# Kernel tuning notes

Hardware: AMD Instinct MI355X
Metric: run time of the kernel (lower is better)

The kernel has to match this reference:

```python
import jax, jax.numpy as jnp
import numpy as np

N_NODES = 100000
N_EDGES = 1600000
F_IN = 128
HID = 128


def setup_inputs() -> dict:
    key = jax.random.key(0)
    ks = jax.random.split(key, 10)
    x = jax.random.normal(ks[0], (N_NODES, F_IN), dtype=jnp.float32)
    edge_index = jax.random.randint(ks[1], (2, N_EDGES), 0, N_NODES, dtype=jnp.int64)
    edge_weight = jax.random.uniform(ks[2], (N_EDGES,), dtype=jnp.float32)
    # Glorot-style params for the three GCNConv layers (conv_mid reused twice)
    W_in = jax.random.normal(ks[3], (F_IN, HID), dtype=jnp.float32) / np.sqrt(F_IN)
    b_in = jnp.zeros((HID,), dtype=jnp.float32)
    W_mid = jax.random.normal(ks[4], (HID, HID), dtype=jnp.float32) / np.sqrt(HID)
    b_mid = jnp.zeros((HID,), dtype=jnp.float32)
    W_fin = jax.random.normal(ks[5], (HID, 1), dtype=jnp.float32) / np.sqrt(HID)
    b_fin = jnp.zeros((1,), dtype=jnp.float32)
    return {"x": x, "edge_index": edge_index, "edge_weight": edge_weight,
            "W_in": W_in, "b_in": b_in, "W_mid": W_mid, "b_mid": b_mid,
            "W_fin": W_fin, "b_fin": b_fin}


def _gcn_norm(edge_index, edge_weight, n_nodes):
    """PyG GCNConv normalization with implicit self-loops (weight 1).
    Returns (edge_norm [E], self_norm [N]) where self_norm = 1/deg."""
    dst = edge_index[1]
    deg = jax.ops.segment_sum(edge_weight, dst, num_segments=n_nodes) + 1.0
    dinv = jnp.where(deg > 0, jax.lax.rsqrt(deg), 0.0)  # deg^-1/2
    edge_norm = dinv[edge_index[0]] * edge_weight * dinv[dst]
    self_norm = dinv * dinv  # self-loop: dinv[i] * 1 * dinv[i]
    return edge_norm, self_norm


def _gcn_conv(x, edge_index, edge_norm, self_norm, W, b, n_nodes):
    h = x @ W  # [N, out]
    msgs = edge_norm[:, None] * h[edge_index[0]]  # [E, out]
    agg = jax.ops.segment_sum(msgs, edge_index[1], num_segments=n_nodes)
    return agg + self_norm[:, None] * h + b


def reference(x, edge_index, edge_weight, W_in, b_in, W_mid, b_mid, W_fin, b_fin):
    n = x.shape[0]
    edge_norm, self_norm = _gcn_norm(edge_index, edge_weight, n)
    h = jax.nn.relu(_gcn_conv(x, edge_index, edge_norm, self_norm, W_in, b_in, n))
    h = jax.nn.relu(_gcn_conv(h, edge_index, edge_norm, self_norm, W_mid, b_mid, n))
    h = jax.nn.relu(_gcn_conv(h, edge_index, edge_norm, self_norm, W_mid, b_mid, n))
    out = _gcn_conv(h, edge_index, edge_norm, self_norm, W_fin, b_fin, n)
    return out  # [N, 1]
```

## Files before the change

kernel.cpp:

```cpp
#include <hip/hip_runtime.h>
#include <stdint.h>

#define N_NODES 100000
#define N_EDGES 1600000
#define F 128
#define CBN 512
#define NCBK 196
#define CHUNK 4096
#define BUFCAP 10240

typedef _Float16 f16;
typedef _Float16 f16x4 __attribute__((ext_vector_type(4)));
typedef _Float16 f16x8 __attribute__((ext_vector_type(8)));
typedef float f32x4 __attribute__((ext_vector_type(4)));

__device__ inline float unpackw(unsigned int p) {
    unsigned short b = (unsigned short)(p & 0x7FFF);
    return (float)__builtin_bit_cast(f16, b);
}


__global__ void k_zero0(int* gcur, unsigned int* edges) {
    int i = threadIdx.x;
    if (i < NCBK) gcur[i] = 0;
    if (i >= 248) edges[(size_t)NCBK * BUFCAP + (i - 248)] = 0u;
}


__launch_bounds__(256)
__global__ void k_binA(const int* __restrict__ ei, const float* __restrict__ w,
                       int* __restrict__ gcur, int2* __restrict__ stage, int e) {
    __shared__ int hist[256];
    __shared__ int bst[257];
    __shared__ int gb[256];
    __shared__ int ls[256];
    __shared__ int rec[CHUNK];
    __shared__ int meta[CHUNK];
    int tid = threadIdx.x;
    int base = blockIdx.x * CHUNK;
    int cnt = min(CHUNK, e - base);
    hist[tid] = 0;
    __syncthreads();

    int ew_[16], mr_[16];
    int nloc = 0;
    if (cnt == CHUNK) {
#pragma unroll
        for (int k = 0; k < 16; k++) {
            int i = base + tid + k * 256;
            int s = ei[i];
            int d = ei[N_EDGES + i];
            f16 hw = (f16)w[i];
            unsigned short wb = __builtin_bit_cast(unsigned short, hw);
            ew_[k] = (int)(((unsigned int)s << 15) | (wb & 0x7FFF));
            int cb = d >> 9;
            int local = d & (CBN - 1);
            int r = atomicAdd(&hist[cb], 1);
            mr_[k] = (cb << 22) | (local << 13) | r;
        }
        nloc = 16;
    } else {
        for (int i = tid; i < cnt; i += 256) {
            int s = ei[base + i];
            int d = ei[N_EDGES + base + i];
            f16 hw = (f16)w[base + i];
            unsigned short wb = __builtin_bit_cast(unsigned short, hw);
            ew_[nloc] = (int)(((unsigned int)s << 15) | (wb & 0x7FFF));
            int cb = d >> 9;
            int local = d & (CBN - 1);
            int r = atomicAdd(&hist[cb], 1);
            mr_[nloc] = (cb << 22) | (local << 13) | r;
            nloc++;
        }
    }
    __syncthreads();
    int v = hist[tid];
    ls[tid] = v;
    __syncthreads();
    for (int off = 1; off < 256; off <<= 1) {
        int t = (tid >= off) ? ls[tid - off] : 0;
        __syncthreads();
        ls[tid] += t;
        __syncthreads();
    }
    bst[tid] = ls[tid] - v;
    if (tid == 255) bst[256] = ls[255];
    __syncthreads();
    for (int k = 0; k < nloc; k++) {
        int m = mr_[k];
        int cb = m >> 22;
        int pos = bst[cb] + (m & 0x1FFF);
        rec[pos] = ew_[k];
        meta[pos] = (cb << 9) | ((m >> 13) & 0x1FF);
    }
    __syncthreads();
    if (tid < NCBK) {
        int c = bst[tid + 1] - bst[tid];
        gb[tid] = c ? atomicAdd(&gcur[tid], c) : 0;
    }
    __syncthreads();
    for (int j = tid; j < cnt; j += 256) {
        int m = meta[j];
        int cb = m >> 9;
        stage[(size_t)cb * BUFCAP + gb[cb] + (j - bst[cb])] = make_int2(m & 511, rec[j]);
    }
}

__launch_bounds__(256)
__global__ void k_binB(const int2* __restrict__ stage, const int* __restrict__ gcur,
                       unsigned int* __restrict__ edges, int2* __restrict__ row2,
                       float* __restrict__ dinv) {
    __shared__ int cnt[CBN];
    __shared__ int ex[CBN + 1];
    __shared__ int cur[CBN];
    __shared__ int ls[256];
    __shared__ unsigned int buf[BUFCAP];
    int tid = threadIdx.x;
    int cb = blockIdx.x;
    int n0 = cb * CBN;
    int nn = min(CBN, N_NODES - n0);
    size_t sbase = (size_t)cb * BUFCAP;
    int ecnt = gcur[cb];
    cnt[tid] = 0;
    cnt[tid + 256] = 0;
    __syncthreads();
    for (int j = tid; j < ecnt; j += 256)
        atomicAdd(&cnt[stage[sbase + j].x], 1);
    __syncthreads();
    int a = cnt[2 * tid], b = cnt[2 * tid + 1];
    int s = a + b;
    ls[tid] = s;
    __syncthreads();
    for (int off = 1; off < 256; off <<= 1) {
        int t = (tid >= off) ? ls[tid - off] : 0;
        __syncthreads();
        ls[tid] += t;
        __syncthreads();
    }
    int bx = ls[tid] - s;
    ex[2 * tid] = bx;
    ex[2 * tid + 1] = bx + a;
    cur[2 * tid] = bx;
    cur[2 * tid + 1] = bx + a;
    if (tid == 255) ex[512] = ls[255];
    __syncthreads();
    for (int l = tid; l < nn; l += 256)
        row2[n0 + l] = make_int2((int)sbase + ex[l], (int)sbase + ex[l + 1]);
    for (int j = tid; j < ecnt; j += 256) {
        int2 r = stage[sbase + j];
        int p = atomicAdd(&cur[r.x], 1);
        buf[p] = (unsigned int)r.y;
    }
    __syncthreads();
    for (int j = tid; j < ecnt; j += 256)
        edges[sbase + j] = buf[j];
    for (int l = tid; l < nn; l += 256) {
        int lo = ex[l];
        int h2 = ex[l + 1];
        float sm = 1.0f;
        for (int j = lo; j < h2; j++) sm += unpackw(buf[j]);
        dinv[n0 + l] = rsqrtf(sm);
    }
}


__global__ void k_wt2(const float* __restrict__ Wa, const float* __restrict__ Wb,
                      f16* __restrict__ Wta, f16* __restrict__ Wtb) {
    const float* W = blockIdx.x ? Wb : Wa;
    f16* Wt = blockIdx.x ? Wtb : Wta;
    int t = threadIdx.x;
#pragma unroll
    for (int it = 0; it < 64; it++) {
        int idx = t + it * 256;
        int k = idx >> 7, n = idx & 127;
        Wt[n * 128 + k] = (f16)W[idx];
    }
}


#define LDK 136

__launch_bounds__(256, 2)
__global__ void k_gemm16(const f16* __restrict__ A, const f16* __restrict__ Wt,
                         const float* __restrict__ dinv, f16* __restrict__ H, int nrows) {
    __shared__ f16 Ws[128 * LDK];
    int tid = threadIdx.x;
    int r0 = blockIdx.x * 128;
    int wave = tid >> 6;
    int lane = tid & 63;
    int lrow = lane & 15;
    int quad = lane >> 4;

    f16x8 a[2][4];
#pragma unroll
    for (int mt = 0; mt < 2; mt++) {
        int row = r0 + wave * 32 + mt * 16 + lrow;
#pragma unroll
        for (int kc = 0; kc < 4; kc++) {
            if (row < nrows)
                a[mt][kc] = *(const f16x8*)&A[(size_t)row * F + kc * 32 + quad * 8];
            else
                a[mt][kc] = (f16x8){};
        }
    }
#pragma unroll
    for (int it = 0; it < 8; it++) {
        int c = tid + it * 256;
        int rw = c >> 4;
        int off = (c & 15) * 8;
        *(f16x8*)&Ws[rw * LDK + off] = *(const f16x8*)&Wt[rw * 128 + off];
    }
    __syncthreads();

    f32x4 acc[2][8] = {};
#pragma unroll
    for (int kc = 0; kc < 4; kc++) {
        f16x8 b[8];
#pragma unroll
        for (int nt = 0; nt < 8; nt++)
            b[nt] = *(const f16x8*)&Ws[(nt * 16 + lrow) * LDK + kc * 32 + quad * 8];
#pragma unroll
        for (int nt = 0; nt < 8; nt++) {
            acc[0][nt] = __builtin_amdgcn_mfma_f32_16x16x32_f16(a[0][kc], b[nt], acc[0][nt], 0, 0, 0);
            acc[1][nt] = __builtin_amdgcn_mfma_f32_16x16x32_f16(a[1][kc], b[nt], acc[1][nt], 0, 0, 0);
        }
    }
    __syncthreads();
#pragma unroll
    for (int mt = 0; mt < 2; mt++) {
#pragma unroll
        for (int r = 0; r < 4; r++) {
            int lr = wave * 32 + mt * 16 + quad * 4 + r;
            int grow = r0 + lr;
            float dv = (grow < nrows) ? dinv[grow] : 0.f;
#pragma unroll
            for (int nt = 0; nt < 8; nt++)
                Ws[lr * 132 + nt * 16 + lrow] = (f16)(acc[mt][nt][r] * dv);
        }
    }
    __syncthreads();
#pragma unroll
    for (int it = 0; it < 8; it++) {
        int c = it * 256 + tid;
        int rw = c >> 4;
        int col = (c & 15) * 8;
        int grow = r0 + rw;
        if (grow < nrows)
            *(f16x8*)&H[(size_t)grow * F + col] = *(const f16x8*)&Ws[rw * 132 + col];
    }
}

__launch_bounds__(256, 2)
__global__ void k_gemmf(const float* __restrict__ A, const f16* __restrict__ Wt,
                        const float* __restrict__ dinv, f16* __restrict__ H, int nrows) {
    __shared__ f16 Ws[128 * LDK];
    int tid = threadIdx.x;
    int r0 = blockIdx.x * 128;
    int wave = tid >> 6;
    int lane = tid & 63;
    int lrow = lane & 15;
    int quad = lane >> 4;

    f16x8 a[2][4];
#pragma unroll
    for (int mt = 0; mt < 2; mt++) {
        int row = r0 + wave * 32 + mt * 16 + lrow;
#pragma unroll
        for (int kc = 0; kc < 4; kc++) {
            if (row < nrows) {
                float4 lo = *(const float4*)&A[(size_t)row * F + kc * 32 + quad * 8];
                float4 hi = *(const float4*)&A[(size_t)row * F + kc * 32 + quad * 8 + 4];
                f16x8 f;
                f[0] = (f16)lo.x; f[1] = (f16)lo.y; f[2] = (f16)lo.z; f[3] = (f16)lo.w;
                f[4] = (f16)hi.x; f[5] = (f16)hi.y; f[6] = (f16)hi.z; f[7] = (f16)hi.w;
                a[mt][kc] = f;
            } else {
                a[mt][kc] = (f16x8){};
            }
        }
    }
#pragma unroll
    for (int it = 0; it < 8; it++) {
        int c = tid + it * 256;
        int rw = c >> 4;
        int off = (c & 15) * 8;
        *(f16x8*)&Ws[rw * LDK + off] = *(const f16x8*)&Wt[rw * 128 + off];
    }
    __syncthreads();

    f32x4 acc[2][8] = {};
#pragma unroll
    for (int kc = 0; kc < 4; kc++) {
        f16x8 b[8];
#pragma unroll
        for (int nt = 0; nt < 8; nt++)
            b[nt] = *(const f16x8*)&Ws[(nt * 16 + lrow) * LDK + kc * 32 + quad * 8];
#pragma unroll
        for (int nt = 0; nt < 8; nt++) {
            acc[0][nt] = __builtin_amdgcn_mfma_f32_16x16x32_f16(a[0][kc], b[nt], acc[0][nt], 0, 0, 0);
            acc[1][nt] = __builtin_amdgcn_mfma_f32_16x16x32_f16(a[1][kc], b[nt], acc[1][nt], 0, 0, 0);
        }
    }
    __syncthreads();
#pragma unroll
    for (int mt = 0; mt < 2; mt++) {
#pragma unroll
        for (int r = 0; r < 4; r++) {
            int lr = wave * 32 + mt * 16 + quad * 4 + r;
            int grow = r0 + lr;
            float dv = (grow < nrows) ? dinv[grow] : 0.f;
#pragma unroll
            for (int nt = 0; nt < 8; nt++)
                Ws[lr * 132 + nt * 16 + lrow] = (f16)(acc[mt][nt][r] * dv);
        }
    }
    __syncthreads();
#pragma unroll
    for (int it = 0; it < 8; it++) {
        int c = it * 256 + tid;
        int rw = c >> 4;
        int col = (c & 15) * 8;
        int grow = r0 + rw;
        if (grow < nrows)
            *(f16x8*)&H[(size_t)grow * F + col] = *(const f16x8*)&Ws[rw * 132 + col];
    }
}


__launch_bounds__(256)
__global__ void k_agg(const f16* __restrict__ H16, const int2* __restrict__ row2,
                      const unsigned int* __restrict__ edges,
                      const float* __restrict__ dinv, const float* __restrict__ bias,
                      f16* __restrict__ out, int n) {
    int node = blockIdx.x * 16 + (threadIdx.x >> 4);
    if (node >= n) return;
    int sub = threadIdx.x & 15;
    int2 rr = row2[node];
    int beg = rr.x, end = rr.y;
    float acc0[8] = {}, acc1[8] = {}, acc2[8] = {}, acc3[8] = {};
    for (int t = (beg & ~3); t < end; t += 8) {
        uint4 ea = *(const uint4*)&edges[t];
        uint4 eb = *(const uint4*)&edges[t + 4];
        unsigned int e[8] = {ea.x, ea.y, ea.z, ea.w, eb.x, eb.y, eb.z, eb.w};
        float w[8];
        unsigned int srcw[8];
#pragma unroll
        for (int k = 0; k < 8; k++) {
            bool live = (t + k >= beg) && (t + k < end);
            w[k] = live ? unpackw(e[k]) : 0.f;
            srcw[k] = (t + k < end) ? e[k] : ea.x;
        }
        f16x8 v[8];
#pragma unroll
        for (int k = 0; k < 8; k++)
            v[k] = *(const f16x8*)&H16[(size_t)(srcw[k] >> 15) * F + sub * 8];
#pragma unroll
        for (int j = 0; j < 8; j++) {
            acc0[j] = fmaf(w[0], (float)v[0][j], acc0[j]);
            acc1[j] = fmaf(w[1], (float)v[1][j], acc1[j]);
            acc2[j] = fmaf(w[2], (float)v[2][j], acc2[j]);
            acc3[j] = fmaf(w[3], (float)v[3][j], acc3[j]);
            acc0[j] = fmaf(w[4], (float)v[4][j], acc0[j]);
            acc1[j] = fmaf(w[5], (float)v[5][j], acc1[j]);
            acc2[j] = fmaf(w[6], (float)v[6][j], acc2[j]);
            acc3[j] = fmaf(w[7], (float)v[7][j], acc3[j]);
        }
    }
    float dd = dinv[node];
    f16x8 h = *(const f16x8*)&H16[(size_t)node * F + sub * 8];
    float4 b0 = *(const float4*)&bias[sub * 8];
    float4 b1 = *(const float4*)&bias[sub * 8 + 4];
    float bb[8] = {b0.x, b0.y, b0.z, b0.w, b1.x, b1.y, b1.z, b1.w};
    f16x8 o;
#pragma unroll
    for (int j = 0; j < 8; j++) {
        float a = acc0[j] + acc1[j] + acc2[j] + acc3[j] + (float)h[j];
        o[j] = (f16)fmaxf(fmaf(dd, a, bb[j]), 0.f);
    }
    *(f16x8*)&out[(size_t)node * F + sub * 8] = o;
}

__launch_bounds__(256)
__global__ void k_agg_dot(const f16* __restrict__ H16, const int2* __restrict__ row2,
                          const unsigned int* __restrict__ edges,
                          const float* __restrict__ dinv, const float* __restrict__ bias,
                          const float* __restrict__ Wf, float* __restrict__ sout, int n) {
    int node = blockIdx.x * 16 + (threadIdx.x >> 4);
    if (node >= n) return;
    int sub = threadIdx.x & 15;
    int2 rr = row2[node];
    int beg = rr.x, end = rr.y;
    float acc0[8] = {}, acc1[8] = {}, acc2[8] = {}, acc3[8] = {};
    for (int t = (beg & ~3); t < end; t += 8) {
        uint4 ea = *(const uint4*)&edges[t];
        uint4 eb = *(const uint4*)&edges[t + 4];
        unsigned int e[8] = {ea.x, ea.y, ea.z, ea.w, eb.x, eb.y, eb.z, eb.w};
        float w[8];
        unsigned int srcw[8];
#pragma unroll
        for (int k = 0; k < 8; k++) {
            bool live = (t + k >= beg) && (t + k < end);
            w[k] = live ? unpackw(e[k]) : 0.f;
            srcw[k] = (t + k < end) ? e[k] : ea.x;
        }
        f16x8 v[8];
#pragma unroll
        for (int k = 0; k < 8; k++)
            v[k] = *(const f16x8*)&H16[(size_t)(srcw[k] >> 15) * F + sub * 8];
#pragma unroll
        for (int j = 0; j < 8; j++) {
            acc0[j] = fmaf(w[0], (float)v[0][j], acc0[j]);
            acc1[j] = fmaf(w[1], (float)v[1][j], acc1[j]);
            acc2[j] = fmaf(w[2], (float)v[2][j], acc2[j]);
            acc3[j] = fmaf(w[3], (float)v[3][j], acc3[j]);
            acc0[j] = fmaf(w[4], (float)v[4][j], acc0[j]);
            acc1[j] = fmaf(w[5], (float)v[5][j], acc1[j]);
            acc2[j] = fmaf(w[6], (float)v[6][j], acc2[j]);
            acc3[j] = fmaf(w[7], (float)v[7][j], acc3[j]);
        }
    }
    float dd = dinv[node];
    f16x8 h = *(const f16x8*)&H16[(size_t)node * F + sub * 8];
    float4 b0 = *(const float4*)&bias[sub * 8];
    float4 b1 = *(const float4*)&bias[sub * 8 + 4];
    float bb[8] = {b0.x, b0.y, b0.z, b0.w, b1.x, b1.y, b1.z, b1.w};
    float4 w0v = *(const float4*)&Wf[sub * 8];
    float4 w1v = *(const float4*)&Wf[sub * 8 + 4];
    float ww[8] = {w0v.x, w0v.y, w0v.z, w0v.w, w1v.x, w1v.y, w1v.z, w1v.w};
    float p = 0.f;
#pragma unroll
    for (int j = 0; j < 8; j++) {
        float a = acc0[j] + acc1[j] + acc2[j] + acc3[j] + (float)h[j];
        p += fmaxf(fmaf(dd, a, bb[j]), 0.f) * ww[j];
    }
    p += __shfl_xor(p, 8, 64);
    p += __shfl_xor(p, 4, 64);
    p += __shfl_xor(p, 2, 64);
    p += __shfl_xor(p, 1, 64);
    if (sub == 0) sout[node] = dd * p;
}

__global__ void k_aggs(const float* __restrict__ s, const int2* __restrict__ row2,
                       const unsigned int* __restrict__ edges,
                       const float* __restrict__ dinv, const float* __restrict__ bf,
                       float* __restrict__ out, int n) {
    int i = blockIdx.x * blockDim.x + threadIdx.x;
    if (i >= n) return;
    float dd = dinv[i];
    float ae = s[i];
    int2 rr = row2[i];
    for (int j = rr.x; j < rr.y; j++) {
        unsigned int p = edges[j];
        ae = fmaf(unpackw(p), s[p >> 15], ae);
    }
    out[i] = fmaf(dd, ae, bf[0]);
}


extern "C" void kernel_launch(void* const* d_in, const int* in_sizes, int n_in,
                              void* d_out, int out_size, void* d_ws, size_t ws_size,
                              hipStream_t stream) {
    const float* x    = (const float*)d_in[0];
    const int*   ei   = (const int*)d_in[1];
    const float* ew   = (const float*)d_in[2];
    const float* Win  = (const float*)d_in[3];
    const float* bin  = (const float*)d_in[4];
    const float* Wmid = (const float*)d_in[5];
    const float* bmid = (const float*)d_in[6];
    const float* Wfin = (const float*)d_in[7];
    const float* bfin = (const float*)d_in[8];
    float* out = (float*)d_out;

    char* ws = (char*)d_ws;
    size_t off = 0;
    auto alloc = [&](size_t bytes) -> char* {
        char* p = ws + off;
        off = (off + bytes + 255) & ~(size_t)255;
        return p;
    };
    float* dinv  = (float*)alloc((size_t)N_NODES * 4);
    int2*  row2  = (int2*)alloc((size_t)N_NODES * 8);
    unsigned int* edges = (unsigned int*)alloc(((size_t)NCBK * BUFCAP + 8) * 4);
    int*   gcur  = (int*)alloc(256 * 4);
    f16*   wtin  = (f16*)alloc(128 * 128 * 2);
    f16*   wtmid = (f16*)alloc(128 * 128 * 2);
    f16*   H16   = (f16*)alloc((size_t)N_NODES * F * 2);
    f16*   AB16  = (f16*)alloc((size_t)N_NODES * F * 2);
    int2* stage = (int2*)H16;
    float* sbuf = (float*)AB16;

    dim3 b256(256);
    int gN = (N_NODES + 255) / 256;
    int gW = (N_NODES + 15) / 16;
    int gG = (N_NODES + 127) / 128;
    int gA = (N_EDGES + CHUNK - 1) / CHUNK;

    hipLaunchKernelGGL(k_zero0, dim3(1), b256, 0, stream, gcur, edges);
    hipLaunchKernelGGL(k_binA, dim3(gA), b256, 0, stream, ei, ew, gcur, stage, N_EDGES);
    hipLaunchKernelGGL(k_binB, dim3(NCBK), b256, 0, stream, stage, gcur, edges, row2, dinv);
    hipLaunchKernelGGL(k_wt2, dim3(2), b256, 0, stream, Win, Wmid, wtin, wtmid);

    hipLaunchKernelGGL(k_gemmf, dim3(gG), b256, 0, stream, x, wtin, dinv, H16, N_NODES);
    hipLaunchKernelGGL(k_agg, dim3(gW), b256, 0, stream, H16, row2, edges, dinv, bin, AB16, N_NODES);
    hipLaunchKernelGGL(k_gemm16, dim3(gG), b256, 0, stream, AB16, wtmid, dinv, H16, N_NODES);
    hipLaunchKernelGGL(k_agg, dim3(gW), b256, 0, stream, H16, row2, edges, dinv, bmid, AB16, N_NODES);
    hipLaunchKernelGGL(k_gemm16, dim3(gG), b256, 0, stream, AB16, wtmid, dinv, H16, N_NODES);
    hipLaunchKernelGGL(k_agg_dot, dim3(gW), b256, 0, stream, H16, row2, edges, dinv, bmid, Wfin, sbuf, N_NODES);
    hipLaunchKernelGGL(k_aggs, dim3(gN), b256, 0, stream, sbuf, row2, edges, dinv, bfin, out, N_NODES);
}
```

Before: 387.4 us.

## Fuse neighbor aggregation with next-layer GEMM and merge zeroing into weight transpose

Replaces the separate aggregation and f16 GEMM kernels with one kernel that aggregates 128 nodes into shared memory, then multiplies by the next layer's weights with MFMA and writes the scaled result. This avoids writing the aggregated activations to global memory and reading them back, and cuts kernel launches. The zeroing kernel is folded into the weight-transpose launch as an extra block. The trade-off is lower gather parallelism: each block processes 128 nodes, with 8 sequential node iterations per thread group, and the fused kernel uses more registers and LDS, which could reduce latency hiding for the irregular gathers.

```diff
diff --git a/kernel.cpp b/kernel.cpp
--- a/kernel.cpp
+++ b/kernel.cpp
@@ -19,12 +19,6 @@
     return (float)__builtin_bit_cast(f16, b);
 }
 
-
-__global__ void k_zero0(int* gcur, unsigned int* edges) {
-    int i = threadIdx.x;
-    if (i < NCBK) gcur[i] = 0;
-    if (i >= 248) edges[(size_t)NCBK * BUFCAP + (i - 248)] = 0u;
-}
 
 
 __launch_bounds__(256)
@@ -165,10 +159,16 @@
 
 
 __global__ void k_wt2(const float* __restrict__ Wa, const float* __restrict__ Wb,
-                      f16* __restrict__ Wta, f16* __restrict__ Wtb) {
+                      f16* __restrict__ Wta, f16* __restrict__ Wtb,
+                      int* __restrict__ gcur, unsigned int* __restrict__ edges) {
+    int t = threadIdx.x;
+    if (blockIdx.x == 2) {
+        if (t < NCBK) gcur[t] = 0;
+        if (t >= 248) edges[(size_t)NCBK * BUFCAP + (t - 248)] = 0u;
+        return;
+    }
     const float* W = blockIdx.x ? Wb : Wa;
     f16* Wt = blockIdx.x ? Wtb : Wta;
-    int t = threadIdx.x;
 #pragma unroll
     for (int it = 0; it < 64; it++) {
         int idx = t + it * 256;
@@ -179,76 +179,6 @@
 
 
 #define LDK 136
-
-__launch_bounds__(256, 2)
-__global__ void k_gemm16(const f16* __restrict__ A, const f16* __restrict__ Wt,
-                         const float* __restrict__ dinv, f16* __restrict__ H, int nrows) {
-    __shared__ f16 Ws[128 * LDK];
-    int tid = threadIdx.x;
-    int r0 = blockIdx.x * 128;
-    int wave = tid >> 6;
-    int lane = tid & 63;
-    int lrow = lane & 15;
-    int quad = lane >> 4;
-
-    f16x8 a[2][4];
-#pragma unroll
-    for (int mt = 0; mt < 2; mt++) {
-        int row = r0 + wave * 32 + mt * 16 + lrow;
-#pragma unroll
-        for (int kc = 0; kc < 4; kc++) {
-            if (row < nrows)
-                a[mt][kc] = *(const f16x8*)&A[(size_t)row * F + kc * 32 + quad * 8];
-            else
-                a[mt][kc] = (f16x8){};
-        }
-    }
-#pragma unroll
-    for (int it = 0; it < 8; it++) {
-        int c = tid + it * 256;
-        int rw = c >> 4;
-        int off = (c & 15) * 8;
-        *(f16x8*)&Ws[rw * LDK + off] = *(const f16x8*)&Wt[rw * 128 + off];
-    }
-    __syncthreads();
-
-    f32x4 acc[2][8] = {};
-#pragma unroll
-    for (int kc = 0; kc < 4; kc++) {
-        f16x8 b[8];
-#pragma unroll
-        for (int nt = 0; nt < 8; nt++)
-            b[nt] = *(const f16x8*)&Ws[(nt * 16 + lrow) * LDK + kc * 32 + quad * 8];
-#pragma unroll
-        for (int nt = 0; nt < 8; nt++) {
-            acc[0][nt] = __builtin_amdgcn_mfma_f32_16x16x32_f16(a[0][kc], b[nt], acc[0][nt], 0, 0, 0);
-            acc[1][nt] = __builtin_amdgcn_mfma_f32_16x16x32_f16(a[1][kc], b[nt], acc[1][nt], 0, 0, 0);
-        }
-    }
-    __syncthreads();
-#pragma unroll
-    for (int mt = 0; mt < 2; mt++) {
-#pragma unroll
-        for (int r = 0; r < 4; r++) {
-            int lr = wave * 32 + mt * 16 + quad * 4 + r;
-            int grow = r0 + lr;
-            float dv = (grow < nrows) ? dinv[grow] : 0.f;
-#pragma unroll
-            for (int nt = 0; nt < 8; nt++)
-                Ws[lr * 132 + nt * 16 + lrow] = (f16)(acc[mt][nt][r] * dv);
-        }
-    }
-    __syncthreads();
-#pragma unroll
-    for (int it = 0; it < 8; it++) {
-        int c = it * 256 + tid;
-        int rw = c >> 4;
-        int col = (c & 15) * 8;
-        int grow = r0 + rw;
-        if (grow < nrows)
-            *(f16x8*)&H[(size_t)grow * F + col] = *(const f16x8*)&Ws[rw * 132 + col];
-    }
-}
 
 __launch_bounds__(256, 2)
 __global__ void k_gemmf(const float* __restrict__ A, const f16* __restrict__ Wt,
@@ -326,58 +256,124 @@
     }
 }
 
-
-__launch_bounds__(256)
-__global__ void k_agg(const f16* __restrict__ H16, const int2* __restrict__ row2,
-                      const unsigned int* __restrict__ edges,
-                      const float* __restrict__ dinv, const float* __restrict__ bias,
-                      f16* __restrict__ out, int n) {
-    int node = blockIdx.x * 16 + (threadIdx.x >> 4);
-    if (node >= n) return;
-    int sub = threadIdx.x & 15;
-    int2 rr = row2[node];
-    int beg = rr.x, end = rr.y;
-    float acc0[8] = {}, acc1[8] = {}, acc2[8] = {}, acc3[8] = {};
-    for (int t = (beg & ~3); t < end; t += 8) {
-        uint4 ea = *(const uint4*)&edges[t];
-        uint4 eb = *(const uint4*)&edges[t + 4];
-        unsigned int e[8] = {ea.x, ea.y, ea.z, ea.w, eb.x, eb.y, eb.z, eb.w};
-        float w[8];
-        unsigned int srcw[8];
-#pragma unroll
-        for (int k = 0; k < 8; k++) {
-            bool live = (t + k >= beg) && (t + k < end);
-            w[k] = live ? unpackw(e[k]) : 0.f;
-            srcw[k] = (t + k < end) ? e[k] : ea.x;
-        }
-        f16x8 v[8];
-#pragma unroll
-        for (int k = 0; k < 8; k++)
-            v[k] = *(const f16x8*)&H16[(size_t)(srcw[k] >> 15) * F + sub * 8];
-#pragma unroll
-        for (int j = 0; j < 8; j++) {
-            acc0[j] = fmaf(w[0], (float)v[0][j], acc0[j]);
-            acc1[j] = fmaf(w[1], (float)v[1][j], acc1[j]);
-            acc2[j] = fmaf(w[2], (float)v[2][j], acc2[j]);
-            acc3[j] = fmaf(w[3], (float)v[3][j], acc3[j]);
-            acc0[j] = fmaf(w[4], (float)v[4][j], acc0[j]);
-            acc1[j] = fmaf(w[5], (float)v[5][j], acc1[j]);
-            acc2[j] = fmaf(w[6], (float)v[6][j], acc2[j]);
-            acc3[j] = fmaf(w[7], (float)v[7][j], acc3[j]);
-        }
-    }
-    float dd = dinv[node];
-    f16x8 h = *(const f16x8*)&H16[(size_t)node * F + sub * 8];
+__launch_bounds__(256, 4)
+__global__ void k_agg_gemm(const f16* __restrict__ Hin, const int2* __restrict__ row2,
+                           const unsigned int* __restrict__ edges,
+                           const float* __restrict__ dinv, const float* __restrict__ bias,
+                           const f16* __restrict__ Wt, f16* __restrict__ Hout, int nrows) {
+    __shared__ f16 S[128 * LDK];
+    int tid = threadIdx.x;
+    int r0 = blockIdx.x * 128;
+    int wave = tid >> 6;
+    int lane = tid & 63;
+    int sub = lane & 15;
+    int quad = lane >> 4;
+
     float4 b0 = *(const float4*)&bias[sub * 8];
     float4 b1 = *(const float4*)&bias[sub * 8 + 4];
     float bb[8] = {b0.x, b0.y, b0.z, b0.w, b1.x, b1.y, b1.z, b1.w};
-    f16x8 o;
-#pragma unroll
-    for (int j = 0; j < 8; j++) {
-        float a = acc0[j] + acc1[j] + acc2[j] + acc3[j] + (float)h[j];
-        o[j] = (f16)fmaxf(fmaf(dd, a, bb[j]), 0.f);
-    }
-    *(f16x8*)&out[(size_t)node * F + sub * 8] = o;
+    for (int it = 0; it < 8; it++) {
+        int l = wave * 32 + it * 4 + quad;
+        int node = r0 + l;
+        f16x8 o = (f16x8){};
+        if (node < nrows) {
+            int2 rr = row2[node];
+            int beg = rr.x, end = rr.y;
+            float acc0[8] = {}, acc1[8] = {}, acc2[8] = {}, acc3[8] = {};
+            for (int t = (beg & ~3); t < end; t += 8) {
+                uint4 ea = *(const uint4*)&edges[t];
+                uint4 eb = *(const uint4*)&edges[t + 4];
+                unsigned int e[8] = {ea.x, ea.y, ea.z, ea.w, eb.x, eb.y, eb.z, eb.w};
+                float w[8];
+                unsigned int srcw[8];
+#pragma unroll
+                for (int k = 0; k < 8; k++) {
+                    bool live = (t + k >= beg) && (t + k < end);
+                    w[k] = live ? unpackw(e[k]) : 0.f;
+                    srcw[k] = (t + k < end) ? e[k] : ea.x;
+                }
+                f16x8 v[8];
+#pragma unroll
+                for (int k = 0; k < 8; k++)
+                    v[k] = *(const f16x8*)&Hin[(size_t)(srcw[k] >> 15) * F + sub * 8];
+#pragma unroll
+                for (int j = 0; j < 8; j++) {
+                    acc0[j] = fmaf(w[0], (float)v[0][j], acc0[j]);
+                    acc1[j] = fmaf(w[1], (float)v[1][j], acc1[j]);
+                    acc2[j] = fmaf(w[2], (float)v[2][j], acc2[j]);
+                    acc3[j] = fmaf(w[3], (float)v[3][j], acc3[j]);
+                    acc0[j] = fmaf(w[4], (float)v[4][j], acc0[j]);
+                    acc1[j] = fmaf(w[5], (float)v[5][j], acc1[j]);
+                    acc2[j] = fmaf(w[6], (float)v[6][j], acc2[j]);
+                    acc3[j] = fmaf(w[7], (float)v[7][j], acc3[j]);
+                }
+            }
+            float dd = dinv[node];
+            f16x8 h = *(const f16x8*)&Hin[(size_t)node * F + sub * 8];
+#pragma unroll
+            for (int j = 0; j < 8; j++) {
+                float a = acc0[j] + acc1[j] + acc2[j] + acc3[j] + (float)h[j];
+                o[j] = (f16)fmaxf(fmaf(dd, a, bb[j]), 0.f);
+            }
+        }
+        *(f16x8*)&S[l * LDK + sub * 8] = o;
+    }
+    __syncthreads();
+
+    f16x8 a[2][4];
+#pragma unroll
+    for (int mt = 0; mt < 2; mt++) {
+        int l = wave * 32 + mt * 16 + sub;
+#pragma unroll
+        for (int kc = 0; kc < 4; kc++)
+            a[mt][kc] = *(const f16x8*)&S[l * LDK + kc * 32 + quad * 8];
+    }
+    __syncthreads();
+#pragma unroll
+    for (int it = 0; it < 8; it++) {
+        int c = tid + it * 256;
+        int rw = c >> 4;
+        int off = (c & 15) * 8;
+        *(f16x8*)&S[rw * LDK + off] = *(const f16x8*)&Wt[rw * 128 + off];
+    }
+    __syncthreads();
+
+    f32x4 acc[2][8] = {};
+#pragma unroll
+    for (int kc = 0; kc < 4; kc++) {
+        f16x8 b[8];
+#pragma unroll
+        for (int nt = 0; nt < 8; nt++)
+            b[nt] = *(const f16x8*)&S[(nt * 16 + sub) * LDK + kc * 32 + quad * 8];
+#pragma unroll
+        for (int nt = 0; nt < 8; nt++) {
+            acc[0][nt] = __builtin_amdgcn_mfma_f32_16x16x32_f16(a[0][kc], b[nt], acc[0][nt], 0, 0, 0);
+            acc[1][nt] = __builtin_amdgcn_mfma_f32_16x16x32_f16(a[1][kc], b[nt], acc[1][nt], 0, 0, 0);
+        }
+    }
+    __syncthreads();
+#pragma unroll
+    for (int mt = 0; mt < 2; mt++) {
+#pragma unroll
+        for (int r = 0; r < 4; r++) {
+            int lr = wave * 32 + mt * 16 + quad * 4 + r;
+            int grow = r0 + lr;
+            float dv = (grow < nrows) ? dinv[grow] : 0.f;
+#pragma unroll
+            for (int nt = 0; nt < 8; nt++)
+                S[lr * 132 + nt * 16 + sub] = (f16)(acc[mt][nt][r] * dv);
+        }
+    }
+    __syncthreads();
+#pragma unroll
+    for (int it = 0; it < 8; it++) {
+        int c = it * 256 + tid;
+        int rw = c >> 4;
+        int col = (c & 15) * 8;
+        int grow = r0 + rw;
+        if (grow < nrows)
+            *(f16x8*)&Hout[(size_t)grow * F + col] = *(const f16x8*)&S[rw * 132 + col];
+    }
 }
 
 __launch_bounds__(256)
@@ -484,10 +480,10 @@
     int*   gcur  = (int*)alloc(256 * 4);
     f16*   wtin  = (f16*)alloc(128 * 128 * 2);
     f16*   wtmid = (f16*)alloc(128 * 128 * 2);
-    f16*   H16   = (f16*)alloc((size_t)N_NODES * F * 2);
-    f16*   AB16  = (f16*)alloc((size_t)N_NODES * F * 2);
-    int2* stage = (int2*)H16;
-    float* sbuf = (float*)AB16;
+    f16*   Ha    = (f16*)alloc((size_t)N_NODES * F * 2);
+    f16*   Hb    = (f16*)alloc((size_t)N_NODES * F * 2);
+    int2* stage = (int2*)Ha;
+    float* sbuf = (float*)Hb;
 
     dim3 b256(256);
     int gN = (N_NODES + 255) / 256;
@@ -495,16 +491,13 @@
     int gG = (N_NODES + 127) / 128;
     int gA = (N_EDGES + CHUNK - 1) / CHUNK;
 
-    hipLaunchKernelGGL(k_zero0, dim3(1), b256, 0, stream, gcur, edges);
+    hipLaunchKernelGGL(k_wt2, dim3(3), b256, 0, stream, Win, Wmid, wtin, wtmid, gcur, edges);
     hipLaunchKernelGGL(k_binA, dim3(gA), b256, 0, stream, ei, ew, gcur, stage, N_EDGES);
     hipLaunchKernelGGL(k_binB, dim3(NCBK), b256, 0, stream, stage, gcur, edges, row2, dinv);
-    hipLaunchKernelGGL(k_wt2, dim3(2), b256, 0, stream, Win, Wmid, wtin, wtmid);
-
-    hipLaunchKernelGGL(k_gemmf, dim3(gG), b256, 0, stream, x, wtin, dinv, H16, N_NODES);
-    hipLaunchKernelGGL(k_agg, dim3(gW), b256, 0, stream, H16, row2, edges, dinv, bin, AB16, N_NODES);
-    hipLaunchKernelGGL(k_gemm16, dim3(gG), b256, 0, stream, AB16, wtmid, dinv, H16, N_NODES);
-    hipLaunchKernelGGL(k_agg, dim3(gW), b256, 0, stream, H16, row2, edges, dinv, bmid, AB16, N_NODES);
-    hipLaunchKernelGGL(k_gemm16, dim3(gG), b256, 0, stream, AB16, wtmid, dinv, H16, N_NODES);
-    hipLaunchKernelGGL(k_agg_dot, dim3(gW), b256, 0, stream, H16, row2, edges, dinv, bmid, Wfin, sbuf, N_NODES);
+
+    hipLaunchKernelGGL(k_gemmf, dim3(gG), b256, 0, stream, x, wtin, dinv, Ha, N_NODES);
+    hipLaunchKernelGGL(k_agg_gemm, dim3(gG), b256, 0, stream, Ha, row2, edges, dinv, bin, wtmid, Hb, N_NODES);
+    hipLaunchKernelGGL(k_agg_gemm, dim3(gG), b256, 0, stream, Hb, row2, edges, dinv, bmid, wtmid, Ha, N_NODES);
+    hipLaunchKernelGGL(k_agg_dot, dim3(gW), b256, 0, stream, Ha, row2, edges, dinv, bmid, Wfin, sbuf, N_NODES);
     hipLaunchKernelGGL(k_aggs, dim3(gN), b256, 0, stream, sbuf, row2, edges, dinv, bfin, out, N_NODES);
 }
```

New measurement: 379.2 us (median of 2 runs). -2.1%, faster.
